# Kernel tuning notes

Measured on AMD Instinct MI355X. Metric: run time of the kernel, lower is better.

## Reference

```python
import jax, jax.numpy as jnp
import numpy as np

MARGIN = 0.4
SCALE = 80.0
NEG_FILL = -1e30  # used instead of -inf for masked logsumexp (keeps grads NaN-free)

N, D, NUM_CLASSES = 8192, 128, 512


def setup_inputs() -> dict:
    key = jax.random.key(0)
    k1, k2 = jax.random.split(key)
    embeds = jax.random.normal(k1, (N, D), dtype=jnp.float32)
    labels = jax.random.randint(k2, (N,), 0, NUM_CLASSES, dtype=jnp.int64)
    return {"embeds": embeds, "labels": labels}


def _masked_lse(terms, mask):
    # stable logsumexp over axis=1 restricted to mask
    t = jnp.where(mask, terms, NEG_FILL)
    m = jnp.max(t, axis=1, keepdims=True)
    return jnp.squeeze(m, 1) + jnp.log(jnp.sum(jnp.exp(t - m), axis=1))


def reference(embeds, labels):
    # L2-normalize embeddings (F.normalize, p=2, dim=1, eps=1e-12)
    norm = jnp.maximum(jnp.linalg.norm(embeds, axis=1, keepdims=True), 1e-12)
    e = embeds / norm
    sim = e @ e.T  # [N, N]

    same = labels[:, None] == labels[None, :]
    eye = jnp.eye(labels.shape[0], dtype=bool)
    pos_mask = same & ~eye          # positives for each anchor (row)
    neg_mask = ~same                # negatives for each anchor

    # alphas are computed under no_grad in the original
    ap_alpha = jax.lax.stop_gradient(jax.nn.relu(1.0 + MARGIN - sim))
    an_alpha = jax.lax.stop_gradient(jax.nn.relu(sim + MARGIN))

    ap_term = -SCALE * ap_alpha * (sim - 1.0 + MARGIN)
    an_term = SCALE * an_alpha * (sim - MARGIN)

    np_cnt = jnp.sum(pos_mask, axis=1)  # positives per anchor
    nn_cnt = jnp.sum(neg_mask, axis=1)  # negatives per anchor
    valid = (np_cnt > 0) & (nn_cnt > 0)

    # All-triplets logsumexp factorizes: LSE over (p,n) pairs of ap_term[p]
    # equals LSE over p + log(num_neg); symmetric for an_term.
    lse_p = _masked_lse(ap_term, pos_mask)
    lse_n = _masked_lse(an_term, neg_mask)
    log_np = jnp.where(valid, jnp.log(np_cnt.astype(sim.dtype)), 0.0)
    log_nn = jnp.where(valid, jnp.log(nn_cnt.astype(sim.dtype)), 0.0)

    loss_i = jax.nn.softplus(lse_p + log_nn + lse_n + log_np)
    loss = jnp.sum(jnp.where(valid, loss_i, 0.0)) / jnp.maximum(
        jnp.sum(valid).astype(sim.dtype), 1.0)
    return loss
```

## Files before the change

kernel.cpp:

```cpp
#include <hip/hip_runtime.h>
#include <hip/hip_bf16.h>

#define NN_ 8192
#define DD_ 128
#define NCLS 512
#define NSPLIT 32
#define JSPLIT (NN_ / NSPLIT)

typedef short bf16x8 __attribute__((ext_vector_type(8)));
typedef float f32x4 __attribute__((ext_vector_type(4)));

union U4 { uint4 u; bf16x8 h; };

#if __has_builtin(__builtin_amdgcn_exp2f)
#define EXP2(x) __builtin_amdgcn_exp2f(x)
#else
#define EXP2(x) __expf((x) * 0.69314718056f)
#endif

#define C1 115.415603f
#define C2 96.9491065f
#define LN2 0.69314718056f

__device__ __forceinline__ unsigned short f2bf(float f) {
    unsigned int u = __float_as_uint(f);
    unsigned int r = (u + 0x7FFFu + ((u >> 16) & 1u)) >> 16;
    return (unsigned short)r;
}


__global__ __launch_bounds__(512) void k_zero(int* __restrict__ hist) {
    hist[threadIdx.x] = 0;
}

__global__ __launch_bounds__(256) void k_hist(const int* __restrict__ labels,
                                              int* __restrict__ hist) {
    int i = blockIdx.x * 256 + threadIdx.x;
    atomicAdd(&hist[labels[i]], 1);
}

__global__ __launch_bounds__(512) void k_scan(const int* __restrict__ hist,
                                              int* __restrict__ start,
                                              int* __restrict__ base) {
    __shared__ int wsum[8];
    int t = threadIdx.x;
    int v = hist[t];
    int x = v;
#pragma unroll
    for (int m = 1; m < 64; m <<= 1) {
        int y = __shfl_up(x, m);
        if ((t & 63) >= m) x += y;
    }
    if ((t & 63) == 63) wsum[t >> 6] = x;
    __syncthreads();
    int w = t >> 6, woff = 0;
#pragma unroll
    for (int k = 0; k < 8; k++)
        if (k < w) woff += wsum[k];
    int excl = woff + x - v;
    start[t] = excl;
    base[t] = excl;
    if (t == 0) start[NCLS] = NN_;
}

__global__ __launch_bounds__(256) void k_scatter(const int* __restrict__ labels,
                                                 int* __restrict__ base,
                                                 int* __restrict__ srcrow,
                                                 int* __restrict__ plab) {
    int row = blockIdx.x * 256 + threadIdx.x;
    int l = labels[row];
    int p = atomicAdd(&base[l], 1);
    srcrow[p] = row;
    plab[p] = l;
}

__global__ __launch_bounds__(256) void k_norm(const float* __restrict__ x,
                                              const int* __restrict__ srcrow,
                                              unsigned short* __restrict__ ebf) {
    int t = threadIdx.x;
    int r16 = t >> 4;
    int g = t & 15;
    int slot = blockIdx.x * 16 + r16;
    int orig = srcrow[slot];
    const float4* xr = (const float4*)(x + (size_t)orig * DD_);
    float4 v0 = xr[g * 2];
    float4 v1 = xr[g * 2 + 1];
    float ss = v0.x * v0.x + v0.y * v0.y + v0.z * v0.z + v0.w * v0.w +
               v1.x * v1.x + v1.y * v1.y + v1.z * v1.z + v1.w * v1.w;
#pragma unroll
    for (int m = 1; m < 16; m <<= 1) ss += __shfl_xor(ss, m);
    float inv = 1.0f / fmaxf(sqrtf(ss), 1e-12f);
    float vs[8] = {v0.x, v0.y, v0.z, v0.w, v1.x, v1.y, v1.z, v1.w};
    unsigned int p[4];
#pragma unroll
    for (int k = 0; k < 4; k++) {
        unsigned short lo = f2bf(vs[2 * k] * inv);
        unsigned short hi = f2bf(vs[2 * k + 1] * inv);
        p[k] = (unsigned int)lo | ((unsigned int)hi << 16);
    }
    uint4 out = {p[0], p[1], p[2], p[3]};
    ((uint4*)ebf)[blockIdx.x * 256 + g * 16 + r16] = out;
}

__global__ __launch_bounds__(512, 4) void k_main(const unsigned short* __restrict__ ebf,
                                                 const int* __restrict__ plab,
                                                 const int* __restrict__ start,
                                                 float* __restrict__ states) {
    __shared__ uint4 bsh[2048];

    const int tid = threadIdx.x;
    const int lane = tid & 63;
    const int wave = tid >> 6;
    const int quad = lane >> 4;
    const int lcol = lane & 15;
    const int rowbase = blockIdx.y * 256 + wave * 32;
    const int jsplit = blockIdx.x;
    const int j0 = jsplit * JSPLIT;

    const uint4* fb = (const uint4*)ebf;

    U4 afr[2][4];
#pragma unroll
    for (int g = 0; g < 2; g++)
#pragma unroll
        for (int kc = 0; kc < 4; kc++)
            afr[g][kc].u = fb[((rowbase >> 4) + g) * 256 + kc * 64 + lane];

    int il[2][4];
#pragma unroll
    for (int g = 0; g < 2; g++)
#pragma unroll
        for (int r = 0; r < 4; r++) il[g][r] = plab[rowbase + g * 16 + quad * 4 + r];

    int labmin = __builtin_amdgcn_readfirstlane(plab[rowbase]);
    int labmax = __builtin_amdgcn_readfirstlane(plab[rowbase + 31]);
    int lo = __builtin_amdgcn_readfirstlane(start[labmin]);
    int hi = __builtin_amdgcn_readfirstlane(start[labmax + 1]);

    float S_an[2][4], m_p[2][4], s_p[2][4], cnt[2][4];
#pragma unroll
    for (int g = 0; g < 2; g++)
#pragma unroll
        for (int r = 0; r < 4; r++) {
            S_an[g][r] = 0.f;
            m_p[g][r] = -1e30f;
            s_p[g][r] = 0.f;
            cnt[g][r] = 0.f;
        }

    {
        const int tb = (j0 >> 4) * 256;
        bsh[tid] = fb[tb + tid];
        bsh[tid + 512] = fb[tb + tid + 512];
    }
    __syncthreads();

    const int NIT = JSPLIT / 64;
    for (int it = 0; it < NIT; ++it) {
        const int cur = it & 1;
        const int jt = j0 + it * 64;
        const bool has = (it + 1 < NIT);

        uint4 stg0, stg1;
        if (has) {
            const int tn = ((jt + 64) >> 4) * 256;
            stg0 = fb[tn + tid];
            stg1 = fb[tn + tid + 512];
        }

        const int bbase = (cur << 10) + lane;

#pragma unroll
        for (int c = 0; c < 4; c++) {
            U4 bf[4];
#pragma unroll
            for (int kc = 0; kc < 4; kc++) bf[kc].u = bsh[bbase + c * 256 + kc * 64];
            f32x4 acc0 = {0.f, 0.f, 0.f, 0.f};
            f32x4 acc1 = {0.f, 0.f, 0.f, 0.f};
#pragma unroll
            for (int kc = 0; kc < 4; kc++) {
                acc0 = __builtin_amdgcn_mfma_f32_16x16x32_bf16(afr[0][kc].h, bf[kc].h, acc0, 0, 0, 0);
                acc1 = __builtin_amdgcn_mfma_f32_16x16x32_bf16(afr[1][kc].h, bf[kc].h, acc1, 0, 0, 0);
            }
            const int jc = jt + c * 16;
            if (jc < hi && jc + 16 > lo) {
                int jl = plab[jc + lcol];
                int j = jc + lcol;
#pragma unroll
                for (int g = 0; g < 2; g++) {
#pragma unroll
                    for (int r = 0; r < 4; r++) {
                        float s = (g == 0) ? acc0[r] : acc1[r];
                        int i = rowbase + g * 16 + quad * 4 + r;
                        bool same = (jl == il[g][r]);
                        float u = fmaxf(s, -0.4f);
                        float e = EXP2(fmaf(u * C1, u, -C1));
                        S_an[g][r] += same ? 0.0f : e;
                        cnt[g][r] += same ? 1.0f : 0.0f;
                        if (same && j != i) {
                            float al = fmaxf(1.4f - s, 0.0f) * (-C1);
                            float tp = al * (s - 0.6f);
                            float mn = fmaxf(m_p[g][r], tp);
                            s_p[g][r] = s_p[g][r] * EXP2(m_p[g][r] - mn) + EXP2(tp - mn);
                            m_p[g][r] = mn;
                        }
                    }
                }
            } else {
#pragma unroll
                for (int r = 0; r < 4; r++) {
                    float u0 = fmaxf(acc0[r], -0.4f);
                    S_an[0][r] += EXP2(fmaf(u0 * C1, u0, -C1));
                    float u1 = fmaxf(acc1[r], -0.4f);
                    S_an[1][r] += EXP2(fmaf(u1 * C1, u1, -C1));
                }
            }
        }

        if (has) {
            bsh[((cur ^ 1) << 10) + tid] = stg0;
            bsh[((cur ^ 1) << 10) + tid + 512] = stg1;
        }
        __syncthreads();
    }

#pragma unroll
    for (int g = 0; g < 2; g++)
#pragma unroll
        for (int r = 0; r < 4; r++) {
#pragma unroll
            for (int m = 1; m < 16; m <<= 1) {
                S_an[g][r] += __shfl_xor(S_an[g][r], m);
                cnt[g][r] += __shfl_xor(cnt[g][r], m);
                float m2 = __shfl_xor(m_p[g][r], m);
                float s2 = __shfl_xor(s_p[g][r], m);
                float mn = fmaxf(m_p[g][r], m2);
                s_p[g][r] = s_p[g][r] * EXP2(m_p[g][r] - mn) + s2 * EXP2(m2 - mn);
                m_p[g][r] = mn;
            }
        }
    if (lcol == 0) {
#pragma unroll
        for (int g = 0; g < 2; g++)
#pragma unroll
            for (int r = 0; r < 4; r++) {
                int i = rowbase + g * 16 + quad * 4 + r;
                float4 st = {m_p[g][r], s_p[g][r], S_an[g][r], cnt[g][r]};
                ((float4*)states)[(size_t)i * NSPLIT + jsplit] = st;
            }
    }
}

__global__ __launch_bounds__(256) void k_fin(const float* __restrict__ states,
                                             float* __restrict__ partials) {
    int i = blockIdx.x * 256 + threadIdx.x;
    float m_p = -1e30f, s_p = 0.f, S_an = 0.f, cnt = 0.f;
#pragma unroll
    for (int k = 0; k < NSPLIT; k++) {
        float4 st = ((const float4*)states)[(size_t)i * NSPLIT + k];
        S_an += st.z;
        cnt += st.w;
        float mn = fmaxf(m_p, st.x);
        s_p = s_p * EXP2(m_p - mn) + st.y * EXP2(st.x - mn);
        m_p = mn;
    }
    int np = (int)cnt - 1;
    int nn = NN_ - (int)cnt;
    float loss = 0.0f, v = 0.0f;
    if (np > 0 && nn > 0 && s_p > 0.f && S_an > 0.f) {
        float lse_p = LN2 * m_p + __logf(s_p);
        float lse_n = 67.2f + __logf(S_an);
        float z = lse_p + lse_n + __logf((float)np) + __logf((float)nn);
        loss = fmaxf(z, 0.0f) + log1pf(__expf(-fabsf(z)));
        v = 1.0f;
    }
#pragma unroll
    for (int m = 1; m < 64; m <<= 1) {
        loss += __shfl_xor(loss, m);
        v += __shfl_xor(v, m);
    }
    if ((threadIdx.x & 63) == 0) {
        int w = (blockIdx.x << 2) | (threadIdx.x >> 6);
        partials[w * 2] = loss;
        partials[w * 2 + 1] = v;
    }
}

__global__ void k_div(const float* __restrict__ partials, float* __restrict__ out) {
    int t = threadIdx.x;
    float loss = partials[t * 2] + partials[(t + 64) * 2];
    float v = partials[t * 2 + 1] + partials[(t + 64) * 2 + 1];
#pragma unroll
    for (int m = 1; m < 64; m <<= 1) {
        loss += __shfl_xor(loss, m);
        v += __shfl_xor(v, m);
    }
    if (t == 0) out[0] = loss / fmaxf(v, 1.0f);
}

extern "C" void kernel_launch(void* const* d_in, const int* in_sizes, int n_in,
                              void* d_out, int out_size, void* d_ws, size_t ws_size,
                              hipStream_t stream) {
    const float* embeds = (const float*)d_in[0];
    const int* labels = (const int*)d_in[1];
    float* out = (float*)d_out;

    char* ws = (char*)d_ws;
    unsigned short* ebf = (unsigned short*)ws;
    float* states = (float*)(ws + 2097152);
    float* partials = (float*)(ws + 6291456);
    int* srcrow = (int*)(ws + 6292480);
    int* plab = (int*)(ws + 6325248);
    int* start = (int*)(ws + 6358016);
    int* base = (int*)(ws + 6360068);
    int* hist = (int*)(ws + 6362116);

    k_zero<<<1, NCLS, 0, stream>>>(hist);
    k_hist<<<NN_ / 256, 256, 0, stream>>>(labels, hist);
    k_scan<<<1, NCLS, 0, stream>>>(hist, start, base);
    k_scatter<<<NN_ / 256, 256, 0, stream>>>(labels, base, srcrow, plab);
    k_norm<<<NN_ / 16, 256, 0, stream>>>(embeds, srcrow, ebf);
    k_main<<<dim3(NSPLIT, NN_ / 256), 512, 0, stream>>>(ebf, plab, start, states);
    k_fin<<<NN_ / 256, 256, 0, stream>>>(states, partials);
    k_div<<<1, 64, 0, stream>>>(partials, out);
}
```

Baseline: 114.3 us.

## Fuse histogram/scan into one kernel and derive class counts from sort offsets

Merges the zero, histogram and scan kernels into a single 1024-thread block that builds the label histogram in shared memory, removing two launches and the global atomics. The per-row same-class counter is dropped from the main loop and its shuffle reduction; k_fin now gets class size from the start offsets instead. The first MFMA of each tile starts from a zero constant rather than zeroing accumulators first. The cost is a serial single-block histogram over 8192 labels with contended shared atomics.

```diff
diff --git a/kernel.cpp b/kernel.cpp
--- a/kernel.cpp
+++ b/kernel.cpp
@@ -29,38 +29,44 @@
 }
 
 
-__global__ __launch_bounds__(512) void k_zero(int* __restrict__ hist) {
-    hist[threadIdx.x] = 0;
-}
-
-__global__ __launch_bounds__(256) void k_hist(const int* __restrict__ labels,
-                                              int* __restrict__ hist) {
-    int i = blockIdx.x * 256 + threadIdx.x;
-    atomicAdd(&hist[labels[i]], 1);
-}
-
-__global__ __launch_bounds__(512) void k_scan(const int* __restrict__ hist,
-                                              int* __restrict__ start,
-                                              int* __restrict__ base) {
+__global__ __launch_bounds__(1024) void k_sorthead(const int* __restrict__ labels,
+                                                   int* __restrict__ start,
+                                                   int* __restrict__ base) {
+    __shared__ int hist[NCLS];
     __shared__ int wsum[8];
     int t = threadIdx.x;
-    int v = hist[t];
+    if (t < NCLS) hist[t] = 0;
+    __syncthreads();
+    int4 la = ((const int4*)labels)[t * 2];
+    int4 lb = ((const int4*)labels)[t * 2 + 1];
+    atomicAdd(&hist[la.x], 1);
+    atomicAdd(&hist[la.y], 1);
+    atomicAdd(&hist[la.z], 1);
+    atomicAdd(&hist[la.w], 1);
+    atomicAdd(&hist[lb.x], 1);
+    atomicAdd(&hist[lb.y], 1);
+    atomicAdd(&hist[lb.z], 1);
+    atomicAdd(&hist[lb.w], 1);
+    __syncthreads();
+    int v = (t < NCLS) ? hist[t] : 0;
     int x = v;
 #pragma unroll
     for (int m = 1; m < 64; m <<= 1) {
         int y = __shfl_up(x, m);
         if ((t & 63) >= m) x += y;
     }
-    if ((t & 63) == 63) wsum[t >> 6] = x;
+    if (t < NCLS && (t & 63) == 63) wsum[t >> 6] = x;
     __syncthreads();
-    int w = t >> 6, woff = 0;
-#pragma unroll
-    for (int k = 0; k < 8; k++)
-        if (k < w) woff += wsum[k];
-    int excl = woff + x - v;
-    start[t] = excl;
-    base[t] = excl;
-    if (t == 0) start[NCLS] = NN_;
+    if (t < NCLS) {
+        int w = t >> 6, woff = 0;
+#pragma unroll
+        for (int k = 0; k < 8; k++)
+            if (k < w) woff += wsum[k];
+        int excl = woff + x - v;
+        start[t] = excl;
+        base[t] = excl;
+        if (t == 0) start[NCLS] = NN_;
+    }
 }
 
 __global__ __launch_bounds__(256) void k_scatter(const int* __restrict__ labels,
@@ -137,7 +143,7 @@
     int lo = __builtin_amdgcn_readfirstlane(start[labmin]);
     int hi = __builtin_amdgcn_readfirstlane(start[labmax + 1]);
 
-    float S_an[2][4], m_p[2][4], s_p[2][4], cnt[2][4];
+    float S_an[2][4], m_p[2][4], s_p[2][4];
 #pragma unroll
     for (int g = 0; g < 2; g++)
 #pragma unroll
@@ -145,8 +151,9 @@
             S_an[g][r] = 0.f;
             m_p[g][r] = -1e30f;
             s_p[g][r] = 0.f;
-            cnt[g][r] = 0.f;
-        }
+        }
+
+    const f32x4 Z = {0.f, 0.f, 0.f, 0.f};
 
     {
         const int tb = (j0 >> 4) * 256;
@@ -175,10 +182,10 @@
             U4 bf[4];
 #pragma unroll
             for (int kc = 0; kc < 4; kc++) bf[kc].u = bsh[bbase + c * 256 + kc * 64];
-            f32x4 acc0 = {0.f, 0.f, 0.f, 0.f};
-            f32x4 acc1 = {0.f, 0.f, 0.f, 0.f};
-#pragma unroll
-            for (int kc = 0; kc < 4; kc++) {
+            f32x4 acc0 = __builtin_amdgcn_mfma_f32_16x16x32_bf16(afr[0][0].h, bf[0].h, Z, 0, 0, 0);
+            f32x4 acc1 = __builtin_amdgcn_mfma_f32_16x16x32_bf16(afr[1][0].h, bf[0].h, Z, 0, 0, 0);
+#pragma unroll
+            for (int kc = 1; kc < 4; kc++) {
                 acc0 = __builtin_amdgcn_mfma_f32_16x16x32_bf16(afr[0][kc].h, bf[kc].h, acc0, 0, 0, 0);
                 acc1 = __builtin_amdgcn_mfma_f32_16x16x32_bf16(afr[1][kc].h, bf[kc].h, acc1, 0, 0, 0);
             }
@@ -196,7 +203,6 @@
                         float u = fmaxf(s, -0.4f);
                         float e = EXP2(fmaf(u * C1, u, -C1));
                         S_an[g][r] += same ? 0.0f : e;
-                        cnt[g][r] += same ? 1.0f : 0.0f;
                         if (same && j != i) {
                             float al = fmaxf(1.4f - s, 0.0f) * (-C1);
                             float tp = al * (s - 0.6f);
@@ -231,7 +237,6 @@
 #pragma unroll
             for (int m = 1; m < 16; m <<= 1) {
                 S_an[g][r] += __shfl_xor(S_an[g][r], m);
-                cnt[g][r] += __shfl_xor(cnt[g][r], m);
                 float m2 = __shfl_xor(m_p[g][r], m);
                 float s2 = __shfl_xor(s_p[g][r], m);
                 float mn = fmaxf(m_p[g][r], m2);
@@ -245,27 +250,30 @@
 #pragma unroll
             for (int r = 0; r < 4; r++) {
                 int i = rowbase + g * 16 + quad * 4 + r;
-                float4 st = {m_p[g][r], s_p[g][r], S_an[g][r], cnt[g][r]};
+                float4 st = {m_p[g][r], s_p[g][r], S_an[g][r], 0.f};
                 ((float4*)states)[(size_t)i * NSPLIT + jsplit] = st;
             }
     }
 }
 
 __global__ __launch_bounds__(256) void k_fin(const float* __restrict__ states,
+                                             const int* __restrict__ plab,
+                                             const int* __restrict__ start,
                                              float* __restrict__ partials) {
     int i = blockIdx.x * 256 + threadIdx.x;
-    float m_p = -1e30f, s_p = 0.f, S_an = 0.f, cnt = 0.f;
+    float m_p = -1e30f, s_p = 0.f, S_an = 0.f;
 #pragma unroll
     for (int k = 0; k < NSPLIT; k++) {
         float4 st = ((const float4*)states)[(size_t)i * NSPLIT + k];
         S_an += st.z;
-        cnt += st.w;
         float mn = fmaxf(m_p, st.x);
         s_p = s_p * EXP2(m_p - mn) + st.y * EXP2(st.x - mn);
         m_p = mn;
     }
-    int np = (int)cnt - 1;
-    int nn = NN_ - (int)cnt;
+    int l = plab[i];
+    int sz = start[l + 1] - start[l];
+    int np = sz - 1;
+    int nn = NN_ - sz;
     float loss = 0.0f, v = 0.0f;
     if (np > 0 && nn > 0 && s_p > 0.f && S_an > 0.f) {
         float lse_p = LN2 * m_p + __logf(s_p);
@@ -313,14 +321,11 @@
     int* plab = (int*)(ws + 6325248);
     int* start = (int*)(ws + 6358016);
     int* base = (int*)(ws + 6360068);
-    int* hist = (int*)(ws + 6362116);
-
-    k_zero<<<1, NCLS, 0, stream>>>(hist);
-    k_hist<<<NN_ / 256, 256, 0, stream>>>(labels, hist);
-    k_scan<<<1, NCLS, 0, stream>>>(hist, start, base);
+
+    k_sorthead<<<1, 1024, 0, stream>>>(labels, start, base);
     k_scatter<<<NN_ / 256, 256, 0, stream>>>(labels, base, srcrow, plab);
     k_norm<<<NN_ / 16, 256, 0, stream>>>(embeds, srcrow, ebf);
     k_main<<<dim3(NSPLIT, NN_ / 256), 512, 0, stream>>>(ebf, plab, start, states);
-    k_fin<<<NN_ / 256, 256, 0, stream>>>(states, partials);
+    k_fin<<<NN_ / 256, 256, 0, stream>>>(states, plab, start, partials);
     k_div<<<1, 64, 0, stream>>>(partials, out);
 }
```

After: 109.1 us. 4.6% less time.
